# Performance work log

Measured on AMD Instinct MI355X. Metric: run time of the kernel, lower is better.

The kernel has to match this reference:

```python
import jax, jax.numpy as jnp
import numpy as np

B = 4096        # number of sets
MAX_N = 64      # max set size (matches max(n) in data)
DIM = 256       # per-element feature dim
W = 32          # weight_dim = sqrt(hidden_dim=1024)


def sinusoid_pe(length, dim):
    # standard transformer sinusoid PE: pe[p,2i]=sin(p/10000^(2i/dim)), pe[p,2i+1]=cos(...)
    pos = jnp.arange(length, dtype=jnp.float32)[:, None]
    i = jnp.arange(dim)[None, :]
    angle = pos / jnp.power(10000.0, (2.0 * (i // 2)).astype(jnp.float32) / dim)
    return jnp.where(i % 2 == 0, jnp.sin(angle), jnp.cos(angle))


def setup_inputs() -> dict:
    key = jax.random.key(0)
    ks = jax.random.split(key, 6)
    # ragged batch: alternating set sizes 32 and 64, 2048 each -> 196608 rows
    counts = np.tile(np.array([32, 64], dtype=np.int64), B // 2)
    batch = jnp.asarray(np.repeat(np.arange(B, dtype=np.int64), counts))
    N = int(counts.sum())
    x = jax.random.normal(ks[0], (N, DIM), dtype=jnp.float32)
    s = 1.0 / np.sqrt(DIM)
    Wk = jax.random.normal(ks[1], (W, DIM), dtype=jnp.float32) * s
    Wv = jax.random.normal(ks[2], (W, DIM), dtype=jnp.float32) * s
    Wq = jax.random.normal(ks[3], (W, DIM), dtype=jnp.float32) * s
    Wmap = jax.random.normal(ks[4], (DIM, W), dtype=jnp.float32) / np.sqrt(W)
    bmap = jax.random.normal(ks[5], (DIM,), dtype=jnp.float32) * 0.01
    return {"x": x, "batch": batch, "Wk": Wk, "Wv": Wv, "Wq": Wq, "Wmap": Wmap, "bmap": bmap}


def reference(x, batch, Wk, Wv, Wq, Wmap, bmap):
    N = x.shape[0]
    # set sizes and within-set positions (vectorized replacement of torch python loops)
    n = jax.ops.segment_sum(jnp.ones((N,), jnp.int32), batch, num_segments=B)
    ptr = jnp.concatenate([jnp.zeros((1,), jnp.int32), jnp.cumsum(n)])[:-1]
    pos_in_set = jnp.arange(N, dtype=jnp.int32) - ptr[batch]

    # --- Encoder ---
    xmat = jnp.zeros((B, MAX_N, DIM), x.dtype).at[batch, pos_in_set].set(x)
    mask = jnp.zeros((B, MAX_N), bool).at[batch, pos_in_set].set(True)
    pe = sinusoid_pe(MAX_N, DIM)                       # [MAX_N, DIM]
    xpos = xmat + pe[None]                             # [B, MAX_N, DIM]
    m = mask[..., None].astype(x.dtype)
    yk = jnp.einsum('bnd,wd->bnw', xpos, Wk) * m       # [B, MAX_N, W]
    yv = jnp.einsum('bnd,wd->bnw', xpos, Wv) * m
    # z_mat[b,i,j] = sum_n yv[b,n,i] * yk[b,n,j]
    z_mat = jnp.einsum('bnj,bni->bij', yk, yv)         # [B, W, W]

    # --- Decoder ---
    query = sinusoid_pe(MAX_N, DIM) @ Wq.T             # [MAX_N, W]
    decoded = jnp.einsum('mk,bkv->bmv', query, z_mat)  # [B, MAX_N, W]
    x_padded = decoded @ Wmap.T + bmap                 # [B, MAX_N, DIM]
    # unpad: gather valid rows back to flat ragged layout
    x_out = x_padded[batch, pos_in_set]                # [N, DIM]
    return (x_out, batch)
```

## Files before the change

kernel.cpp:

```cpp
#include <hip/hip_runtime.h>
#include <math.h>

#define N_SETS 4096
#define SETS_PER_BLOCK 4
#define GRID_MAIN (N_SETS / SETS_PER_BLOCK)

typedef _Float16 f16;
typedef __attribute__((ext_vector_type(8))) _Float16 f16x8;
typedef __attribute__((ext_vector_type(4))) _Float16 f16x4;
typedef __attribute__((ext_vector_type(4))) float     f32x4;

#define WS_PE    0
#define WS_QH    65536
#define WS_WKV   69632
#define WS_WMAPH 102400
#define WS_PEH   118784
#define WS_PTR   151552

__global__ void k_aux1(const int* __restrict__ batch, float* __restrict__ out2,
                       int* __restrict__ ptr, int N, float* __restrict__ pe) {
    int blk = blockIdx.x;
    if (blk < 768) {
        int i = blk * 256 + threadIdx.x;
        if (i >= N) return;
        int b = batch[i];
        out2[i] = (float)b;
        if (i == 0 || batch[i - 1] != b) ptr[b] = i;
        if (i == N - 1) ptr[N_SETS] = N;
    } else {
        int idx = (blk - 768) * 256 + threadIdx.x;
        int p = idx >> 8, i = idx & 255;
        float e   = (float)(2 * (i / 2)) / 256.0f;
        float inv = powf(10000.0f, -e);
        float ang = (float)p * inv;
        pe[idx] = (i & 1) ? cosf(ang) : sinf(ang);
    }
}

__global__ void k_aux2(const float* __restrict__ Wk, const float* __restrict__ Wv,
                       const float* __restrict__ Wq, const float* __restrict__ Wmap,
                       const float* __restrict__ pe, f16* __restrict__ wkv,
                       f16* __restrict__ wmaph, f16* __restrict__ peh,
                       f16* __restrict__ qh) {
    int blk = blockIdx.x;
    if (blk < 96) {
        int idx = blk * 256 + threadIdx.x;
        if (idx < 16384) {
            int j = idx >> 8, d = idx & 255;
            float v = (j < 32) ? Wk[j * 256 + d] : Wv[(j - 32) * 256 + d];
            wkv[idx] = (f16)v;
        } else {
            int i2 = idx - 16384;
            wmaph[i2] = (f16)Wmap[i2];
        }
    } else if (blk < 160) {
        int idx = (blk - 96) * 256 + threadIdx.x;
        peh[idx] = (f16)pe[idx];
    } else {
        int idx = (blk - 160) * 256 + threadIdx.x;
        int pos = idx >> 5, k = idx & 31;
        const float* pr = pe + pos * 256;
        const float* wr = Wq + k * 256;
        float s = 0.f;
        for (int d = 0; d < 256; d += 4) {
            float4 a = *(const float4*)(pr + d);
            float4 b = *(const float4*)(wr + d);
            s += a.x * b.x + a.y * b.y + a.z * b.z + a.w * b.w;
        }
        qh[idx] = (f16)s;
    }
}

__global__ __launch_bounds__(256, 2) void k_main(
        const float* __restrict__ x,     const f16* __restrict__ wkv,
        const f16* __restrict__ wmaph,   const f16* __restrict__ qh,
        const f16* __restrict__ peh,     const float* __restrict__ bmap,
        const int* __restrict__ ptr,     float* __restrict__ out) {
    __shared__ char lds[77824];
    char* wmh  = lds + 32768;
    char* dsh  = lds + 73728;

    const int t    = threadIdx.x;
    const int wv   = t >> 6;
    const int l15  = t & 15;
    const int lhi  = (t & 63) >> 4;
    const int arow = 16 * wv + l15;
    const int swz7 = (l15 & 7) << 4;

    int pv[SETS_PER_BLOCK + 1];
    #pragma unroll
    for (int i = 0; i <= SETS_PER_BLOCK; ++i)
        pv[i] = ptr[blockIdx.x * SETS_PER_BLOCK + i];

    #pragma unroll
    for (int i2 = 0; i2 < 8; ++i2) {
        int c = t + 256 * i2;
        int j = c >> 5, d0 = (c & 31) * 8;
        *(f16x8*)(lds + ((j * 512 + d0 * 2) ^ ((j & 7) << 4))) =
            *(const f16x8*)(wkv + j * 256 + d0);
    }
    #pragma unroll
    for (int i2 = 0; i2 < 4; ++i2) {
        int c = t + 256 * i2;
        int d = c >> 2, v0 = (c & 3) * 8;
        *(f16x8*)(wmh + ((d * 64 + v0 * 2) ^ ((d & 7) << 4))) =
            *(const f16x8*)(wmaph + d * 32 + v0);
    }
    f16x8 pef[8];
    #pragma unroll
    for (int ks = 0; ks < 8; ++ks)
        pef[ks] = *(const f16x8*)(peh + arow * 256 + ks * 32 + lhi * 8);
    const f16x8 qreg = *(const f16x8*)(qh + arow * 32 + lhi * 8);
    float bm[16];
    #pragma unroll
    for (int nt = 0; nt < 16; ++nt) bm[nt] = bmap[16 * nt + l15];

    float4 xf[16];
    {
        const int s0 = pv[0], n0 = pv[1] - pv[0];
        if (arow < n0) {
            const float* xr = x + (size_t)(s0 + arow) * 256 + lhi * 8;
            #pragma unroll
            for (int ks = 0; ks < 8; ++ks) {
                xf[2 * ks]     = *(const float4*)(xr + ks * 32);
                xf[2 * ks + 1] = *(const float4*)(xr + ks * 32 + 4);
            }
        }
    }
    __syncthreads();

    auto gemm2 = [&](int jj, char* yb) {
        const int n2 = pv[jj + 1] - pv[jj];
        const int nks = ((n2 + 31) & ~31) >> 5;
        const int it = wv >> 1, jt = wv & 1;
        f32x4 zacc = {0.f, 0.f, 0.f, 0.f};
        const int ca = 32 + 16 * it + l15, cb = 16 * jt + l15;
        for (int ks = 0; ks < nks; ++ks) {
            const int r2 = ks * 64 + lhi * 16;
            f16x8 av = *(const f16x8*)(yb + ((ca * 128 + r2) ^ swz7));
            f16x8 bk = *(const f16x8*)(yb + ((cb * 128 + r2) ^ swz7));
            zacc = __builtin_amdgcn_mfma_f32_16x16x32_f16(av, bk, zacc, 0, 0, 0);
        }
        const int zc = 16 * jt + l15, zr0 = 16 * it + lhi * 4;
        f16x4 h4;
        #pragma unroll
        for (int q = 0; q < 4; ++q) h4[q] = (f16)zacc[q];
        *(f16x4*)(lds + 65536 + jj * 2048 + ((zc * 64 + zr0 * 2) ^ ((l15 & 3) << 4))) = h4;
    };

    #pragma unroll
    for (int j = 0; j < SETS_PER_BLOCK; ++j) {
        char* ycur = lds + 49152 + (j & 1) * 8192;
        if (j > 0) gemm2(j - 1, lds + 49152 + ((j - 1) & 1) * 8192);

        const int s = pv[j], n = pv[j + 1] - s;
        const int n32 = (n + 31) & ~31;

        f16x8 areg[8];
        if (arow < n) {
            #pragma unroll
            for (int ks = 0; ks < 8; ++ks) {
                float4 a = xf[2 * ks], a2 = xf[2 * ks + 1];
                f16x8 h;
                h[0]=(f16)a.x;  h[1]=(f16)a.y;  h[2]=(f16)a.z;  h[3]=(f16)a.w;
                h[4]=(f16)a2.x; h[5]=(f16)a2.y; h[6]=(f16)a2.z; h[7]=(f16)a2.w;
                areg[ks] = h + pef[ks];
            }
        } else {
            #pragma unroll
            for (int ks = 0; ks < 8; ++ks) {
                f16x8 h;
                #pragma unroll
                for (int ii = 0; ii < 8; ++ii) h[ii] = (f16)0.f;
                areg[ks] = h;
            }
        }
        if (j + 1 < SETS_PER_BLOCK) {
            const int s1 = pv[j + 1], n1 = pv[j + 2] - pv[j + 1];
            if (arow < n1) {
                const float* xr1 = x + (size_t)(s1 + arow) * 256 + lhi * 8;
                #pragma unroll
                for (int ks = 0; ks < 8; ++ks) {
                    xf[2 * ks]     = *(const float4*)(xr1 + ks * 32);
                    xf[2 * ks + 1] = *(const float4*)(xr1 + ks * 32 + 4);
                }
            }
        }

        if (16 * wv < n32) {
            f32x4 acc[4];
            #pragma unroll
            for (int nt = 0; nt < 4; ++nt) acc[nt] = (f32x4){0.f, 0.f, 0.f, 0.f};
            #pragma unroll
            for (int ks = 0; ks < 8; ++ks) {
                #pragma unroll
                for (int nt = 0; nt < 4; ++nt) {
                    f16x8 bf = *(const f16x8*)(lds +
                        (((16 * nt + l15) * 512 + ks * 64 + lhi * 16) ^ swz7));
                    acc[nt] = __builtin_amdgcn_mfma_f32_16x16x32_f16(areg[ks], bf, acc[nt], 0, 0, 0);
                }
            }
            const int row0 = 16 * wv + lhi * 4;
            #pragma unroll
            for (int nt = 0; nt < 4; ++nt) {
                const int col = 16 * nt + l15;
                f16x4 h4;
                #pragma unroll
                for (int q = 0; q < 4; ++q) h4[q] = (f16)acc[nt][q];
                *(f16x4*)(ycur + ((col * 128 + row0 * 2) ^ swz7)) = h4;
            }
        }
        __syncthreads();
    }
    gemm2(SETS_PER_BLOCK - 1, lds + 49152 + ((SETS_PER_BLOCK - 1) & 1) * 8192);
    __syncthreads();

    #pragma unroll
    for (int j = 0; j < SETS_PER_BLOCK; ++j) {
        const int s = pv[j], n = pv[j + 1] - s;
        if (16 * wv >= n) continue;
        char* zsh = lds + 65536 + j * 2048;
        const int k2 = lhi * 16;

        {
            f16x8 bz0 = *(const f16x8*)(zsh + ((l15 * 64 + k2) ^ ((l15 & 3) << 4)));
            f16x8 bz1 = *(const f16x8*)(zsh + (((16 + l15) * 64 + k2) ^ ((l15 & 3) << 4)));
            f32x4 dd0 = {0.f, 0.f, 0.f, 0.f}, dd1 = {0.f, 0.f, 0.f, 0.f};
            dd0 = __builtin_amdgcn_mfma_f32_16x16x32_f16(qreg, bz0, dd0, 0, 0, 0);
            dd1 = __builtin_amdgcn_mfma_f32_16x16x32_f16(qreg, bz1, dd1, 0, 0, 0);
            #pragma unroll
            for (int q = 0; q < 4; ++q) {
                const int m = 16 * wv + lhi * 4 + q;
                *(f16*)(dsh + ((m * 64 + l15 * 2) ^ ((m & 7) << 4)))        = (f16)dd0[q];
                *(f16*)(dsh + ((m * 64 + (16 + l15) * 2) ^ ((m & 7) << 4))) = (f16)dd1[q];
            }
        }
        {
            f16x8 ad = *(const f16x8*)(dsh + (((16 * wv + l15) * 64 + k2) ^ swz7));
            const int row0 = 16 * wv + lhi * 4;
            float* ob = out + (size_t)s * 256;
            #pragma unroll
            for (int nt = 0; nt < 16; ++nt) {
                const int dcol = 16 * nt + l15;
                f16x8 bw = *(const f16x8*)(wmh + ((dcol * 64 + k2) ^ swz7));
                f32x4 o = {0.f, 0.f, 0.f, 0.f};
                o = __builtin_amdgcn_mfma_f32_16x16x32_f16(ad, bw, o, 0, 0, 0);
                #pragma unroll
                for (int q = 0; q < 4; ++q)
                    ob[(size_t)(row0 + q) * 256 + dcol] = o[q] + bm[nt];
            }
        }
    }
}

extern "C" void kernel_launch(void* const* d_in, const int* in_sizes, int n_in,
                              void* d_out, int out_size, void* d_ws, size_t ws_size,
                              hipStream_t stream) {
    const float* x    = (const float*)d_in[0];
    const int*   batch= (const int*)  d_in[1];
    const float* Wk   = (const float*)d_in[2];
    const float* Wv   = (const float*)d_in[3];
    const float* Wq   = (const float*)d_in[4];
    const float* Wmap = (const float*)d_in[5];
    const float* bmap = (const float*)d_in[6];
    float* out = (float*)d_out;

    const int N = in_sizes[1];
    float* pe    = (float*)((char*)d_ws + WS_PE);
    f16*   qh    = (f16*)  ((char*)d_ws + WS_QH);
    f16*   wkv   = (f16*)  ((char*)d_ws + WS_WKV);
    f16*   wmaph = (f16*)  ((char*)d_ws + WS_WMAPH);
    f16*   peh   = (f16*)  ((char*)d_ws + WS_PEH);
    int*   ptr   = (int*)  ((char*)d_ws + WS_PTR);
    float* out2  = out + (size_t)N * 256;

    k_aux1<<<832, 256, 0, stream>>>(batch, out2, ptr, N, pe);
    k_aux2<<<168, 256, 0, stream>>>(Wk, Wv, Wq, Wmap, pe, wkv, wmaph, peh, qh);
    k_main<<<GRID_MAIN, 256, 0, stream>>>(x, wkv, wmaph, qh, peh, bmap, ptr, out);
}
```

Before: 117.0 us.

## Split fused kernel into encoder and per-warp decoder kernels via global z buffer

Splits the fused encode+decode kernel into two. The encoder runs a persistent-style grid of 768 blocks, each looping over a contiguous range of sets and writing z (as f16) to a workspace buffer. A separate decoder kernel assigns one set per wavefront, keeps Wmap and query fragments in registers, and specialises the loop count on set size. This aims to raise occupancy through smaller LDS per kernel and to balance decode work across waves, at the cost of an extra launch and a global round-trip for z.

After: 146.5 us. +25.2%, slower.

```diff
diff --git a/kernel.cpp b/kernel.cpp
--- a/kernel.cpp
+++ b/kernel.cpp
@@ -2,13 +2,16 @@
 #include <math.h>
 
 #define N_SETS 4096
-#define SETS_PER_BLOCK 4
-#define GRID_MAIN (N_SETS / SETS_PER_BLOCK)
+#define ENC_BLOCKS 768
+#define DEC_SPB 4
+#define DEC_BLOCKS (N_SETS / DEC_SPB)
 
 typedef _Float16 f16;
 typedef __attribute__((ext_vector_type(8))) _Float16 f16x8;
 typedef __attribute__((ext_vector_type(4))) _Float16 f16x4;
 typedef __attribute__((ext_vector_type(4))) float     f32x4;
+
+template <int V> struct IC { static constexpr int value = V; };
 
 #define WS_PE    0
 #define WS_QH    65536
@@ -16,6 +19,7 @@
 #define WS_WMAPH 102400
 #define WS_PEH   118784
 #define WS_PTR   151552
+#define WS_ZT    169984
 
 __global__ void k_aux1(const int* __restrict__ batch, float* __restrict__ out2,
                        int* __restrict__ ptr, int N, float* __restrict__ pe) {
@@ -71,14 +75,11 @@
     }
 }
 
-__global__ __launch_bounds__(256, 2) void k_main(
-        const float* __restrict__ x,     const f16* __restrict__ wkv,
-        const f16* __restrict__ wmaph,   const f16* __restrict__ qh,
-        const f16* __restrict__ peh,     const float* __restrict__ bmap,
-        const int* __restrict__ ptr,     float* __restrict__ out) {
-    __shared__ char lds[77824];
-    char* wmh  = lds + 32768;
-    char* dsh  = lds + 73728;
+__global__ __launch_bounds__(256, 3) void k_enc(
+        const float* __restrict__ x,   const f16* __restrict__ wkv,
+        const f16* __restrict__ peh,   const int* __restrict__ ptr,
+        f16* __restrict__ zt) {
+    __shared__ char lds[49152];
 
     const int t    = threadIdx.x;
     const int wv   = t >> 6;
@@ -87,10 +88,9 @@
     const int arow = 16 * wv + l15;
     const int swz7 = (l15 & 7) << 4;
 
-    int pv[SETS_PER_BLOCK + 1];
-    #pragma unroll
-    for (int i = 0; i <= SETS_PER_BLOCK; ++i)
-        pv[i] = ptr[blockIdx.x * SETS_PER_BLOCK + i];
+    const int g0  = (blockIdx.x * N_SETS) / ENC_BLOCKS;
+    const int g1  = ((blockIdx.x + 1) * N_SETS) / ENC_BLOCKS;
+    const int cnt = g1 - g0;
 
     #pragma unroll
     for (int i2 = 0; i2 < 8; ++i2) {
@@ -99,25 +99,14 @@
         *(f16x8*)(lds + ((j * 512 + d0 * 2) ^ ((j & 7) << 4))) =
             *(const f16x8*)(wkv + j * 256 + d0);
     }
-    #pragma unroll
-    for (int i2 = 0; i2 < 4; ++i2) {
-        int c = t + 256 * i2;
-        int d = c >> 2, v0 = (c & 3) * 8;
-        *(f16x8*)(wmh + ((d * 64 + v0 * 2) ^ ((d & 7) << 4))) =
-            *(const f16x8*)(wmaph + d * 32 + v0);
-    }
     f16x8 pef[8];
     #pragma unroll
     for (int ks = 0; ks < 8; ++ks)
         pef[ks] = *(const f16x8*)(peh + arow * 256 + ks * 32 + lhi * 8);
-    const f16x8 qreg = *(const f16x8*)(qh + arow * 32 + lhi * 8);
-    float bm[16];
-    #pragma unroll
-    for (int nt = 0; nt < 16; ++nt) bm[nt] = bmap[16 * nt + l15];
 
     float4 xf[16];
     {
-        const int s0 = pv[0], n0 = pv[1] - pv[0];
+        const int s0 = ptr[g0], n0 = ptr[g0 + 1] - ptr[g0];
         if (arow < n0) {
             const float* xr = x + (size_t)(s0 + arow) * 256 + lhi * 8;
             #pragma unroll
@@ -129,8 +118,7 @@
     }
     __syncthreads();
 
-    auto gemm2 = [&](int jj, char* yb) {
-        const int n2 = pv[jj + 1] - pv[jj];
+    auto gemm2 = [&](int g2, int n2, char* yb) {
         const int nks = ((n2 + 31) & ~31) >> 5;
         const int it = wv >> 1, jt = wv & 1;
         f32x4 zacc = {0.f, 0.f, 0.f, 0.f};
@@ -141,20 +129,19 @@
             f16x8 bk = *(const f16x8*)(yb + ((cb * 128 + r2) ^ swz7));
             zacc = __builtin_amdgcn_mfma_f32_16x16x32_f16(av, bk, zacc, 0, 0, 0);
         }
-        const int zc = 16 * jt + l15, zr0 = 16 * it + lhi * 4;
         f16x4 h4;
         #pragma unroll
         for (int q = 0; q < 4; ++q) h4[q] = (f16)zacc[q];
-        *(f16x4*)(lds + 65536 + jj * 2048 + ((zc * 64 + zr0 * 2) ^ ((l15 & 3) << 4))) = h4;
+        const int zv = 16 * jt + l15, zk0 = 16 * it + lhi * 4;
+        *(f16x4*)(zt + (size_t)g2 * 1024 + zv * 32 + zk0) = h4;
     };
 
-    #pragma unroll
-    for (int j = 0; j < SETS_PER_BLOCK; ++j) {
-        char* ycur = lds + 49152 + (j & 1) * 8192;
-        if (j > 0) gemm2(j - 1, lds + 49152 + ((j - 1) & 1) * 8192);
-
-        const int s = pv[j], n = pv[j + 1] - s;
+    int gprev = 0, nprev = 0;
+    for (int j = 0; j < cnt; ++j) {
+        const int g = g0 + j;
+        const int s = ptr[g], n = ptr[g + 1] - s;
         const int n32 = (n + 31) & ~31;
+        char* ycur = lds + 32768 + (j & 1) * 8192;
 
         f16x8 areg[8];
         if (arow < n) {
@@ -175,8 +162,8 @@
                 areg[ks] = h;
             }
         }
-        if (j + 1 < SETS_PER_BLOCK) {
-            const int s1 = pv[j + 1], n1 = pv[j + 2] - pv[j + 1];
+        if (j + 1 < cnt) {
+            const int s1 = ptr[g + 1], n1 = ptr[g + 2] - ptr[g + 1];
             if (arow < n1) {
                 const float* xr1 = x + (size_t)(s1 + arow) * 256 + lhi * 8;
                 #pragma unroll
@@ -186,6 +173,7 @@
                 }
             }
         }
+        if (j > 0) gemm2(gprev, nprev, lds + 32768 + ((j - 1) & 1) * 8192);
 
         if (16 * wv < n32) {
             f32x4 acc[4];
@@ -211,46 +199,74 @@
             }
         }
         __syncthreads();
-    }
-    gemm2(SETS_PER_BLOCK - 1, lds + 49152 + ((SETS_PER_BLOCK - 1) & 1) * 8192);
-    __syncthreads();
-
-    #pragma unroll
-    for (int j = 0; j < SETS_PER_BLOCK; ++j) {
-        const int s = pv[j], n = pv[j + 1] - s;
-        if (16 * wv >= n) continue;
-        char* zsh = lds + 65536 + j * 2048;
-        const int k2 = lhi * 16;
-
-        {
-            f16x8 bz0 = *(const f16x8*)(zsh + ((l15 * 64 + k2) ^ ((l15 & 3) << 4)));
-            f16x8 bz1 = *(const f16x8*)(zsh + (((16 + l15) * 64 + k2) ^ ((l15 & 3) << 4)));
-            f32x4 dd0 = {0.f, 0.f, 0.f, 0.f}, dd1 = {0.f, 0.f, 0.f, 0.f};
-            dd0 = __builtin_amdgcn_mfma_f32_16x16x32_f16(qreg, bz0, dd0, 0, 0, 0);
-            dd1 = __builtin_amdgcn_mfma_f32_16x16x32_f16(qreg, bz1, dd1, 0, 0, 0);
+        gprev = g; nprev = n;
+    }
+    gemm2(gprev, nprev, lds + 32768 + ((cnt - 1) & 1) * 8192);
+}
+
+__global__ __launch_bounds__(256, 3) void k_dec(
+        const f16* __restrict__ zt,    const f16* __restrict__ wmaph,
+        const f16* __restrict__ qh,    const float* __restrict__ bmap,
+        const int* __restrict__ ptr,   float* __restrict__ out) {
+    __shared__ char lds[16384];
+    const int t    = threadIdx.x;
+    const int wid  = t >> 6;
+    const int l15  = t & 15;
+    const int lhi  = (t & 63) >> 4;
+    const int swz7 = (l15 & 7) << 4;
+    char* dsh = lds + wid * 4096;
+
+    f16x8 bw[16];
+    float bm[16];
+    #pragma unroll
+    for (int nt = 0; nt < 16; ++nt) {
+        bw[nt] = *(const f16x8*)(wmaph + (16 * nt + l15) * 32 + lhi * 8);
+        bm[nt] = bmap[16 * nt + l15];
+    }
+    f16x8 qf[4];
+    #pragma unroll
+    for (int mt = 0; mt < 4; ++mt)
+        qf[mt] = *(const f16x8*)(qh + (16 * mt + l15) * 32 + lhi * 8);
+
+    const int g = blockIdx.x * DEC_SPB + wid;
+    const int s = ptr[g], n = ptr[g + 1] - s;
+
+    const f16* ztg = zt + (size_t)g * 1024;
+    const f16x8 bz0 = *(const f16x8*)(ztg + l15 * 32 + lhi * 8);
+    const f16x8 bz1 = *(const f16x8*)(ztg + (16 + l15) * 32 + lhi * 8);
+
+    float* ob = out + (size_t)s * 256;
+
+    auto decode = [&](auto nmtc) {
+        constexpr int NMT = decltype(nmtc)::value;
+        #pragma unroll
+        for (int mt = 0; mt < NMT; ++mt) {
+            f32x4 d0 = {0.f, 0.f, 0.f, 0.f}, d1 = {0.f, 0.f, 0.f, 0.f};
+            d0 = __builtin_amdgcn_mfma_f32_16x16x32_f16(qf[mt], bz0, d0, 0, 0, 0);
+            d1 = __builtin_amdgcn_mfma_f32_16x16x32_f16(qf[mt], bz1, d1, 0, 0, 0);
             #pragma unroll
             for (int q = 0; q < 4; ++q) {
-                const int m = 16 * wv + lhi * 4 + q;
-                *(f16*)(dsh + ((m * 64 + l15 * 2) ^ ((m & 7) << 4)))        = (f16)dd0[q];
-                *(f16*)(dsh + ((m * 64 + (16 + l15) * 2) ^ ((m & 7) << 4))) = (f16)dd1[q];
-            }
-        }
-        {
-            f16x8 ad = *(const f16x8*)(dsh + (((16 * wv + l15) * 64 + k2) ^ swz7));
-            const int row0 = 16 * wv + lhi * 4;
-            float* ob = out + (size_t)s * 256;
+                const int m = 16 * mt + lhi * 4 + q;
+                *(f16*)(dsh + ((m * 64 + l15 * 2) ^ ((m & 7) << 4)))        = (f16)d0[q];
+                *(f16*)(dsh + ((m * 64 + (16 + l15) * 2) ^ ((m & 7) << 4))) = (f16)d1[q];
+            }
+        }
+        #pragma unroll
+        for (int mt = 0; mt < NMT; ++mt) {
+            f16x8 ad = *(const f16x8*)(dsh + (((16 * mt + l15) * 64 + lhi * 16) ^ swz7));
+            const int row0 = 16 * mt + lhi * 4;
             #pragma unroll
             for (int nt = 0; nt < 16; ++nt) {
-                const int dcol = 16 * nt + l15;
-                f16x8 bw = *(const f16x8*)(wmh + ((dcol * 64 + k2) ^ swz7));
                 f32x4 o = {0.f, 0.f, 0.f, 0.f};
-                o = __builtin_amdgcn_mfma_f32_16x16x32_f16(ad, bw, o, 0, 0, 0);
+                o = __builtin_amdgcn_mfma_f32_16x16x32_f16(ad, bw[nt], o, 0, 0, 0);
                 #pragma unroll
                 for (int q = 0; q < 4; ++q)
-                    ob[(size_t)(row0 + q) * 256 + dcol] = o[q] + bm[nt];
-            }
-        }
-    }
+                    ob[(size_t)(row0 + q) * 256 + 16 * nt + l15] = o[q] + bm[nt];
+            }
+        }
+    };
+    if (n > 32) decode(IC<4>{});
+    else        decode(IC<2>{});
 }
 
 extern "C" void kernel_launch(void* const* d_in, const int* in_sizes, int n_in,
@@ -272,9 +288,11 @@
     f16*   wmaph = (f16*)  ((char*)d_ws + WS_WMAPH);
     f16*   peh   = (f16*)  ((char*)d_ws + WS_PEH);
     int*   ptr   = (int*)  ((char*)d_ws + WS_PTR);
+    f16*   zt    = (f16*)  ((char*)d_ws + WS_ZT);
     float* out2  = out + (size_t)N * 256;
 
     k_aux1<<<832, 256, 0, stream>>>(batch, out2, ptr, N, pe);
     k_aux2<<<168, 256, 0, stream>>>(Wk, Wv, Wq, Wmap, pe, wkv, wmaph, peh, qh);
-    k_main<<<GRID_MAIN, 256, 0, stream>>>(x, wkv, wmaph, qh, peh, bmap, ptr, out);
-}
+    k_enc<<<ENC_BLOCKS, 256, 0, stream>>>(x, wkv, peh, ptr, zt);
+    k_dec<<<DEC_BLOCKS, 256, 0, stream>>>(zt, wmaph, qh, bmap, ptr, out);
+}
```
